# Kernel tuning notes

Measured on AMD Instinct MI355X. Metric: run time of the kernel, lower is better.

## Reference

```python
import jax, jax.numpy as jnp
import numpy as np

HEADS = 12
D_MODEL = 768
D_K = D_MODEL // HEADS


def setup_inputs() -> dict:
    key = jax.random.key(0)
    ks = jax.random.split(key, 5)
    B, S = 2, 2048
    scale = 1.0 / np.sqrt(D_MODEL)
    return {
        "q": jax.random.normal(ks[0], (B, S, D_MODEL), dtype=jnp.float32),
        "k": jax.random.normal(ks[1], (B, S, D_MODEL), dtype=jnp.float32),
        "v": jax.random.normal(ks[2], (B, S, D_MODEL), dtype=jnp.float32),
        "Wk": jax.random.normal(ks[3], (D_MODEL, D_MODEL), dtype=jnp.float32) * scale,
        "bk": jnp.zeros((D_MODEL,), dtype=jnp.float32),
        "Wo": jax.random.normal(ks[4], (D_MODEL, D_MODEL), dtype=jnp.float32) * scale,
        "bo": jnp.zeros((D_MODEL,), dtype=jnp.float32),
    }


def reference(q, k, v, Wk, bk, Wo, bo):
    B, S, _ = q.shape
    # NOTE: faithful to source bug: q, k, v ALL projected with k_linear.
    def proj(x):
        y = x @ Wk.T + bk                    # [B,S,D]
        return y.reshape(B, -1, HEADS, D_K).transpose(0, 2, 1, 3)  # [B,H,S,Dk]

    qh, kh, vh = proj(q), proj(k), proj(v)
    scores = jnp.einsum('bhsd,bhtd->bhst', qh, kh) / jnp.sqrt(jnp.float32(D_K))
    attn = jax.nn.softmax(scores, axis=-1)   # dropout is identity in eval
    out = jnp.einsum('bhst,bhtd->bhsd', attn, vh)
    concat = out.transpose(0, 2, 1, 3).reshape(B, -1, D_MODEL)
    return concat @ Wo.T + bo
```

## Files before the change

kernel.cpp:

```cpp
#include <hip/hip_runtime.h>
#include <hip/hip_bf16.h>
#include <stddef.h>

#define HEADS 12
#define DM 768
#define DK 64
#define SEQ 2048
#define NB 2
#define WSZ (DM * DM)
#define QSCALE 0.18033688011112043f

typedef __attribute__((ext_vector_type(8))) short short8;
typedef __attribute__((ext_vector_type(4))) float f32x4;

#define MFMA16(A, B, C) __builtin_amdgcn_mfma_f32_16x16x32_bf16((A), (B), (C), 0, 0, 0)

__device__ __forceinline__ unsigned short f2bf(float x) {
  union { float f; unsigned u; } c;
  c.f = x;
  unsigned r = (c.u + 0x7FFFu + ((c.u >> 16) & 1u)) >> 16;
  return (unsigned short)r;
}
__device__ __forceinline__ float bf2f(unsigned short h) {
  union { float f; unsigned u; } c;
  c.u = ((unsigned)h) << 16;
  return c.f;
}

__device__ __forceinline__ void async16(const void* g, void* l) {
  __builtin_amdgcn_global_load_lds(
      (const __attribute__((address_space(1))) void*)g,
      (__attribute__((address_space(3))) void*)l, 16, 0, 0);
}

__device__ __forceinline__ void splitpk(float a, float b, unsigned& hu, unsigned& lu) {
  union { __hip_bfloat162 v; unsigned u; } c;
  c.v = __float22bfloat162_rn(make_float2(a, b));
  hu = c.u;
  const float ra = a - bf2f((unsigned short)(hu & 0xFFFFu));
  const float rb = b - bf2f((unsigned short)(hu >> 16));
  c.v = __float22bfloat162_rn(make_float2(ra, rb));
  lu = c.u;
}
__device__ __forceinline__ unsigned pk2bf(float a, float b) {
  union { __hip_bfloat162 v; unsigned u; } c;
  c.v = __float22bfloat162_rn(make_float2(a, b));
  return c.u;
}


__global__ __launch_bounds__(256) void prep_split(
    const float* __restrict__ q, const float* __restrict__ k,
    const float* __restrict__ v, const float* __restrict__ Wk,
    const float* __restrict__ Wo, unsigned short* __restrict__ xq,
    unsigned short* __restrict__ xk, unsigned short* __restrict__ xv,
    unsigned short* __restrict__ wkh, unsigned short* __restrict__ wkl,
    unsigned short* __restrict__ woh, unsigned short* __restrict__ wol) {
  __shared__ __align__(16) unsigned short Lh[64 * 136];
  __shared__ __align__(16) unsigned short Ll[64 * 136];
  const int tid = threadIdx.x;
  int id = blockIdx.x;
  const float* S;
  unsigned short *H, *L = nullptr;
  int RT, RT16;
  if (id < 1152) {
    S = (id < 384) ? q : (id < 768) ? k : v;
    H = (id < 384) ? xq : (id < 768) ? xk : xv;
    id = id % 384; RT = 64; RT16 = 256;
  } else if (id < 1224) {
    S = Wk; H = wkh; L = wkl; id -= 1152; RT = 12; RT16 = 48;
  } else {
    S = Wo; H = woh; L = wol; id -= 1224; RT = 12; RT16 = 48;
  }
  const int rb = id % RT, kb = id / RT;
  const int mlane = tid >> 4;
  const int klane = (tid & 15) * 8;

#pragma unroll
  for (int rr = 0; rr < 4; ++rr) {
    const int m = rr * 16 + mlane;
    const float* src = &S[(size_t)(rb * 64 + m) * DM + kb * 128 + klane];
    float a[8];
    *(float4*)&a[0] = *(const float4*)&src[0];
    *(float4*)&a[4] = *(const float4*)&src[4];
    if (L) {
      unsigned hu[4], lu[4];
#pragma unroll
      for (int u = 0; u < 4; ++u) splitpk(a[2 * u], a[2 * u + 1], hu[u], lu[u]);
      *(uint4*)&Lh[m * 136 + klane] = *(uint4*)&hu[0];
      *(uint4*)&Ll[m * 136 + klane] = *(uint4*)&lu[0];
    } else {
      unsigned hu[4];
#pragma unroll
      for (int u = 0; u < 4; ++u) hu[u] = pk2bf(a[2 * u], a[2 * u + 1]);
      *(uint4*)&Lh[m * 136 + klane] = *(uint4*)&hu[0];
    }
  }
  __syncthreads();

  const int t = tid >> 4;
  const int ktp = t >> 2, mtp = t & 3;
  const size_t gt = ((size_t)(kb * 4 + ktp) * RT16 + (rb * 4 + mtp)) * 512;
#pragma unroll
  for (int i = 0; i < 4; ++i) {
    const int c = i * 16 + (tid & 15);
    const int lsrc = (mtp * 16 + (tid & 15)) * 136 + ktp * 32 + i * 8;
    *(uint4*)&H[gt + c * 8] = *(uint4*)&Lh[lsrc];
    if (L) *(uint4*)&L[gt + c * 8] = *(uint4*)&Ll[lsrc];
  }
}

__global__ __launch_bounds__(256, 3) void gemm_proj(
    const unsigned short* __restrict__ Xq, const unsigned short* __restrict__ Xk,
    const unsigned short* __restrict__ Xv, const unsigned short* __restrict__ Bh_,
    const unsigned short* __restrict__ Bl_, const float* __restrict__ bias,
    unsigned short* __restrict__ q_h, unsigned short* __restrict__ q_l,
    unsigned short* __restrict__ k_h, unsigned short* __restrict__ vt_h) {
  __shared__ __align__(16) unsigned short Ash[8 * 512];
  __shared__ __align__(16) unsigned short Bsh[6 * 512];
  __shared__ __align__(16) unsigned short Bsl[6 * 512];

  const int tid = threadIdx.x, z = blockIdx.z;
  const unsigned short* __restrict__ A = (z == 0) ? Xq : (z == 1) ? Xk : Xv;
  const int id = blockIdx.x;
  const int mt0 = (id & 31) * 8, nt0 = (id >> 5) * 6;
  const int lane = tid & 63, wv = tid >> 6;
  const int l15 = lane & 15, quad = lane >> 4;
  const int wm = (wv >> 1) * 4, wn = (wv & 1) * 3;
  const int lx = lane * 8;

  f32x4 acc[4][3];
#pragma unroll
  for (int i = 0; i < 4; ++i)
#pragma unroll
    for (int j = 0; j < 3; ++j) acc[i][j] = (f32x4){0.f, 0.f, 0.f, 0.f};

  for (int kt = 0; kt < 24; ++kt) {
    __syncthreads();
    async16(&A[((size_t)kt * 256 + mt0 + wv) * 512 + lx], &Ash[wv * 512]);
    async16(&A[((size_t)kt * 256 + mt0 + wv + 4) * 512 + lx], &Ash[(wv + 4) * 512]);
    async16(&Bh_[((size_t)kt * 48 + nt0 + wv) * 512 + lx], &Bsh[wv * 512]);
    async16(&Bl_[((size_t)kt * 48 + nt0 + wv) * 512 + lx], &Bsl[wv * 512]);
    if (wv < 2)
      async16(&Bh_[((size_t)kt * 48 + nt0 + 4 + wv) * 512 + lx], &Bsh[(4 + wv) * 512]);
    else
      async16(&Bl_[((size_t)kt * 48 + nt0 + 2 + wv) * 512 + lx], &Bsl[(2 + wv) * 512]);
    __syncthreads();

    short8 bh8[3], bl8[3];
#pragma unroll
    for (int nt = 0; nt < 3; ++nt) {
      bh8[nt] = *(const short8*)&Bsh[(wn + nt) * 512 + lx];
      bl8[nt] = *(const short8*)&Bsl[(wn + nt) * 512 + lx];
    }
#pragma unroll
    for (int mt = 0; mt < 4; ++mt) {
      const short8 ah8 = *(const short8*)&Ash[(wm + mt) * 512 + lx];
#pragma unroll
      for (int nt = 0; nt < 3; ++nt) {
        acc[mt][nt] = MFMA16(ah8, bh8[nt], acc[mt][nt]);
        acc[mt][nt] = MFMA16(ah8, bl8[nt], acc[mt][nt]);
      }
    }
  }

#pragma unroll
  for (int mt = 0; mt < 4; ++mt)
#pragma unroll
    for (int nt = 0; nt < 3; ++nt) {
      const int n = (nt0 + wn + nt) * 16 + l15;
      const float bv = bias[n];
      const int hh = n >> 6, dk = n & 63;
#pragma unroll
      for (int j = 0; j < 4; ++j) {
        const int m = (mt0 + wm + mt) * 16 + quad * 4 + j;
        const int b = m >> 11, t = m & 2047;
        const int bh = b * HEADS + hh;
        if (z == 0) {
          const float y = (acc[mt][nt][j] + bv) * QSCALE;
          const unsigned short yh = f2bf(y);
          const int a = (bh * SEQ + t) * DK + dk;
          q_h[a] = yh;
          q_l[a] = f2bf(y - bf2f(yh));
        } else if (z == 1) {
          const int a = bh * 131072 + (dk >> 5) * 65536 + (t >> 4) * 512 +
                        (((dk & 31) >> 3) * 16 + (t & 15)) * 8 + (dk & 7);
          k_h[a] = f2bf(acc[mt][nt][j] + bv);
        } else {
          const int a = bh * 131072 + (t >> 5) * 2048 + (dk >> 4) * 512 +
                        (((t & 31) >> 3) * 16 + (dk & 15)) * 8 + (t & 7);
          vt_h[a] = f2bf(acc[mt][nt][j] + bv);
        }
      }
    }
}

__global__ __launch_bounds__(256, 2) void gemm_out(
    const unsigned short* __restrict__ Ah_, const unsigned short* __restrict__ Al_,
    const unsigned short* __restrict__ Bh_, const unsigned short* __restrict__ Bl_,
    const float* __restrict__ bias, float* __restrict__ outF) {
  __shared__ __align__(16) unsigned short Ash[4 * 512];
  __shared__ __align__(16) unsigned short Asl[4 * 512];
  __shared__ __align__(16) unsigned short Bsh[6 * 512];
  __shared__ __align__(16) unsigned short Bsl[6 * 512];

  const int tid = threadIdx.x, id = blockIdx.x;
  const int mt0 = (id & 63) * 4, nt0 = (id >> 6) * 6;
  const int lane = tid & 63, wv = tid >> 6;
  const int l15 = lane & 15, quad = lane >> 4;
  const int wm = (wv >> 1) * 2, wn = (wv & 1) * 3;
  const int lx = lane * 8;

  f32x4 acc[2][3];
#pragma unroll
  for (int i = 0; i < 2; ++i)
#pragma unroll
    for (int j = 0; j < 3; ++j) acc[i][j] = (f32x4){0.f, 0.f, 0.f, 0.f};

  for (int kt = 0; kt < 24; ++kt) {
    __syncthreads();
    async16(&Ah_[((size_t)kt * 256 + mt0 + wv) * 512 + lx], &Ash[wv * 512]);
    async16(&Al_[((size_t)kt * 256 + mt0 + wv) * 512 + lx], &Asl[wv * 512]);
    async16(&Bh_[((size_t)kt * 48 + nt0 + wv) * 512 + lx], &Bsh[wv * 512]);
    async16(&Bl_[((size_t)kt * 48 + nt0 + wv) * 512 + lx], &Bsl[wv * 512]);
    if (wv < 2)
      async16(&Bh_[((size_t)kt * 48 + nt0 + 4 + wv) * 512 + lx], &Bsh[(4 + wv) * 512]);
    else
      async16(&Bl_[((size_t)kt * 48 + nt0 + 2 + wv) * 512 + lx], &Bsl[(2 + wv) * 512]);
    __syncthreads();

    short8 bh8[3], bl8[3];
#pragma unroll
    for (int nt = 0; nt < 3; ++nt) {
      bh8[nt] = *(const short8*)&Bsh[(wn + nt) * 512 + lx];
      bl8[nt] = *(const short8*)&Bsl[(wn + nt) * 512 + lx];
    }
#pragma unroll
    for (int mt = 0; mt < 2; ++mt) {
      const short8 ah8 = *(const short8*)&Ash[(wm + mt) * 512 + lx];
      const short8 al8 = *(const short8*)&Asl[(wm + mt) * 512 + lx];
#pragma unroll
      for (int nt = 0; nt < 3; ++nt) {
        acc[mt][nt] = MFMA16(ah8, bh8[nt], acc[mt][nt]);
        acc[mt][nt] = MFMA16(al8, bh8[nt], acc[mt][nt]);
        acc[mt][nt] = MFMA16(ah8, bl8[nt], acc[mt][nt]);
      }
    }
  }

#pragma unroll
  for (int mt = 0; mt < 2; ++mt)
#pragma unroll
    for (int nt = 0; nt < 3; ++nt) {
      const int n = (nt0 + wn + nt) * 16 + l15;
      const float bv = bias[n];
#pragma unroll
      for (int j = 0; j < 4; ++j) {
        const int m = (mt0 + wm + mt) * 16 + quad * 4 + j;
        outF[(size_t)m * DM + n] = acc[mt][nt][j] + bv;
      }
    }
}

__global__ __launch_bounds__(256, 3) void attn_mfma(
    const unsigned short* __restrict__ q_h, const unsigned short* __restrict__ q_l,
    const unsigned short* __restrict__ k_h, const unsigned short* __restrict__ vt_h,
    unsigned short* __restrict__ cch, unsigned short* __restrict__ ccl) {
  __shared__ __align__(16) unsigned short Ks[8 * 512];
  __shared__ __align__(16) unsigned short Vs[8 * 512];
  __shared__ __align__(16) unsigned short Ps[4 * 1024];
  __shared__ float Osh[64 * 68];
  __shared__ float Lred[4][2][16];

  const int tid = threadIdx.x, lane = tid & 63, wv = tid >> 6;
  const int l15 = lane & 15, quad = lane >> 4;
  const int qh = wv & 1, th = wv >> 1;
  const int id = blockIdx.x;
  const int bh = id % 24, q0 = (id / 24) << 6;
  const int lx = lane * 8;

  short8 Qf[2][2][2];
#pragma unroll
  for (int qt = 0; qt < 2; ++qt)
#pragma unroll
    for (int ks = 0; ks < 2; ++ks) {
      const int off =
          (bh * SEQ + q0 + qh * 32 + qt * 16 + l15) * DK + ks * 32 + quad * 8;
      Qf[qt][ks][0] = *(const short8*)&q_h[off];
      Qf[qt][ks][1] = *(const short8*)&q_l[off];
    }

  f32x4 O[2][4];
#pragma unroll
  for (int i = 0; i < 2; ++i)
#pragma unroll
    for (int j = 0; j < 4; ++j) O[i][j] = (f32x4){0.f, 0.f, 0.f, 0.f};
  float lsum[2] = {0.f, 0.f};

  const size_t kbase = (size_t)bh * 131072;
  const size_t vbase = (size_t)bh * 131072;

  for (int t0 = 0; t0 < SEQ; t0 += 64) {
    __syncthreads();
    async16(&k_h[kbase + ((size_t)(t0 >> 4) + wv) * 512 + lx], &Ks[wv * 512]);
    async16(&k_h[kbase + 65536 + ((size_t)(t0 >> 4) + wv) * 512 + lx],
            &Ks[(4 + wv) * 512]);
    async16(&vt_h[vbase + (size_t)(t0 >> 5) * 2048 + wv * 512 + lx],
            &Vs[wv * 512]);
    async16(&vt_h[vbase + ((size_t)(t0 >> 5) + 1) * 2048 + wv * 512 + lx],
            &Vs[(4 + wv) * 512]);
    __syncthreads();

    f32x4 St[2][2];
#pragma unroll
    for (int i = 0; i < 2; ++i)
#pragma unroll
      for (int j = 0; j < 2; ++j) St[i][j] = (f32x4){0.f, 0.f, 0.f, 0.f};
#pragma unroll
    for (int ks = 0; ks < 2; ++ks)
#pragma unroll
      for (int tt = 0; tt < 2; ++tt) {
        const short8 kh8 = *(const short8*)&Ks[(ks * 4 + th * 2 + tt) * 512 + lx];
#pragma unroll
        for (int qt = 0; qt < 2; ++qt) {
          St[tt][qt] = MFMA16(kh8, Qf[qt][ks][0], St[tt][qt]);
          St[tt][qt] = MFMA16(kh8, Qf[qt][ks][1], St[tt][qt]);
        }
      }

#pragma unroll
    for (int tt = 0; tt < 2; ++tt)
#pragma unroll
      for (int qt = 0; qt < 2; ++qt) {
        const float p0 = __builtin_amdgcn_exp2f(fminf(St[tt][qt][0], 40.f));
        const float p1 = __builtin_amdgcn_exp2f(fminf(St[tt][qt][1], 40.f));
        const float p2 = __builtin_amdgcn_exp2f(fminf(St[tt][qt][2], 40.f));
        const float p3 = __builtin_amdgcn_exp2f(fminf(St[tt][qt][3], 40.f));
        lsum[qt] += (p0 + p1) + (p2 + p3);
        unsigned pk[2];
        pk[0] = pk2bf(p0, p1);
        pk[1] = pk2bf(p2, p3);
        *(uint2*)&Ps[wv * 1024 + qt * 512 +
                     ((2 * tt + (quad >> 1)) * 16 + l15) * 8 + (quad & 1) * 4] =
            *(uint2*)&pk[0];
      }
    asm volatile("s_waitcnt lgkmcnt(0)" ::: "memory");

    short8 pf[2];
#pragma unroll
    for (int qt = 0; qt < 2; ++qt)
      pf[qt] = *(const short8*)&Ps[wv * 1024 + qt * 512 + lx];
#pragma unroll
    for (int nt = 0; nt < 4; ++nt) {
      const short8 vh8 = *(const short8*)&Vs[(th * 4 + nt) * 512 + lx];
      O[0][nt] = MFMA16(pf[0], vh8, O[0][nt]);
      O[1][nt] = MFMA16(pf[1], vh8, O[1][nt]);
    }
  }

#pragma unroll
  for (int qt = 0; qt < 2; ++qt) {
    float l = lsum[qt];
    l += __shfl_xor(l, 16);
    l += __shfl_xor(l, 32);
    if (quad == 0) Lred[wv][qt][l15] = l;
  }
  __syncthreads();
  if (th == 1) {
#pragma unroll
    for (int qt = 0; qt < 2; ++qt)
#pragma unroll
      for (int nt = 0; nt < 4; ++nt)
#pragma unroll
        for (int j = 0; j < 4; ++j)
          Osh[(qh * 32 + qt * 16 + quad * 4 + j) * 68 + nt * 16 + l15] =
              O[qt][nt][j];
  }
  __syncthreads();
  if (th == 0) {
    const int b = bh / HEADS, hh = bh % HEADS;
#pragma unroll
    for (int qt = 0; qt < 2; ++qt)
#pragma unroll
      for (int j = 0; j < 4; ++j) {
        const int qloc = qh * 32 + qt * 16 + quad * 4 + j;
        const float inv = 1.0f / (Lred[wv][qt][quad * 4 + j] +
                                  Lred[wv + 2][qt][quad * 4 + j]);
        const int m = b * SEQ + q0 + qloc;
#pragma unroll
        for (int nt = 0; nt < 4; ++nt) {
          const float y = (O[qt][nt][j] + Osh[qloc * 68 + nt * 16 + l15]) * inv;
          const int kk = hh * 64 + nt * 16 + l15;
          const int a = ((kk >> 5) * 256 + (m >> 4)) * 512 +
                        (((kk & 31) >> 3) * 16 + (m & 15)) * 8 + (kk & 7);
          const unsigned short yh = f2bf(y);
          cch[a] = yh;
          ccl[a] = f2bf(y - bf2f(yh));
        }
      }
  }
}

extern "C" void kernel_launch(void* const* d_in, const int* in_sizes, int n_in,
                              void* d_out, int out_size, void* d_ws,
                              size_t ws_size, hipStream_t stream) {
  const float* q = (const float*)d_in[0];
  const float* k = (const float*)d_in[1];
  const float* v = (const float*)d_in[2];
  const float* Wk = (const float*)d_in[3];
  const float* bk = (const float*)d_in[4];
  const float* Wo = (const float*)d_in[5];
  const float* bo = (const float*)d_in[6];
  float* out = (float*)d_out;

  const size_t SZ = (size_t)NB * SEQ * DM;
  unsigned short* ws16 = (unsigned short*)d_ws;
  unsigned short* xq = ws16;
  unsigned short* xk = ws16 + SZ;
  unsigned short* xv = ws16 + 2 * SZ;
  unsigned short* cch = xq;
  unsigned short* ccl = xk;
  unsigned short* qp_h = ws16 + 3 * SZ;
  unsigned short* qp_l = ws16 + 4 * SZ;
  unsigned short* kp = ws16 + 5 * SZ;
  unsigned short* vtp = ws16 + 6 * SZ;
  unsigned short* wkh = ws16 + 7 * SZ;
  unsigned short* wkl = wkh + WSZ;
  unsigned short* woh = wkl + WSZ;
  unsigned short* wol = woh + WSZ;

  prep_split<<<dim3(1296), 256, 0, stream>>>(q, k, v, Wk, Wo, xq, xk, xv, wkh,
                                             wkl, woh, wol);
  gemm_proj<<<dim3(256, 1, 3), 256, 0, stream>>>(xq, xk, xv, wkh, wkl, bk,
                                                 qp_h, qp_l, kp, vtp);
  attn_mfma<<<dim3(768), 256, 0, stream>>>(qp_h, qp_l, kp, vtp, cch, ccl);
  gemm_out<<<dim3(512), 256, 0, stream>>>(cch, ccl, woh, wol, bo, out);
}
```

Before: 203.7 us.

## Double-buffer K/V tiles in attention loop with async prefetch and MFMA priority

The attention loop now keeps two LDS buffers for K/V. It issues the async copy for the next tile before computing the current one, so global loads overlap with MFMA and softmax work. The full __syncthreads pair is replaced by a vmcnt wait plus raw barriers, and s_setprio raises wave priority around the MFMA blocks. The staging buffers are unioned with the output-reduction scratch to keep LDS usage bounded. The last iteration issues a wasted prefetch that wraps to tile 0, and correctness now depends on the hand-placed waitcnt/barrier ordering.

```diff
diff --git a/kernel.cpp b/kernel.cpp
--- a/kernel.cpp
+++ b/kernel.cpp
@@ -266,10 +266,11 @@
     const unsigned short* __restrict__ q_h, const unsigned short* __restrict__ q_l,
     const unsigned short* __restrict__ k_h, const unsigned short* __restrict__ vt_h,
     unsigned short* __restrict__ cch, unsigned short* __restrict__ ccl) {
-  __shared__ __align__(16) unsigned short Ks[8 * 512];
-  __shared__ __align__(16) unsigned short Vs[8 * 512];
+  __shared__ __align__(16) union {
+    unsigned short stage[2][16 * 512];
+    float osh[64 * 68];
+  } sm;
   __shared__ __align__(16) unsigned short Ps[4 * 1024];
-  __shared__ float Osh[64 * 68];
   __shared__ float Lred[4][2][16];
 
   const int tid = threadIdx.x, lane = tid & 63, wv = tid >> 6;
@@ -297,25 +298,38 @@
     for (int j = 0; j < 4; ++j) O[i][j] = (f32x4){0.f, 0.f, 0.f, 0.f};
   float lsum[2] = {0.f, 0.f};
 
-  const size_t kbase = (size_t)bh * 131072;
-  const size_t vbase = (size_t)bh * 131072;
-
+  const unsigned short* __restrict__ kbh = k_h + (size_t)bh * 131072;
+  const unsigned short* __restrict__ vbh = vt_h + (size_t)bh * 131072;
+
+#define STAGE(T0S, BUF)                                                          \
+  do {                                                                           \
+    unsigned short* Ksb_ = &sm.stage[(BUF)][0];                                  \
+    unsigned short* Vsb_ = &sm.stage[(BUF)][8 * 512];                            \
+    async16(&kbh[((size_t)((T0S) >> 4) + wv) * 512 + lx], &Ksb_[wv * 512]);      \
+    async16(&kbh[65536 + ((size_t)((T0S) >> 4) + wv) * 512 + lx],                \
+            &Ksb_[(4 + wv) * 512]);                                              \
+    async16(&vbh[(size_t)((T0S) >> 5) * 2048 + wv * 512 + lx],                   \
+            &Vsb_[wv * 512]);                                                    \
+    async16(&vbh[((size_t)((T0S) >> 5) + 1) * 2048 + wv * 512 + lx],             \
+            &Vsb_[(4 + wv) * 512]);                                              \
+  } while (0)
+
+  STAGE(0, 0);
+  int cur = 0;
   for (int t0 = 0; t0 < SEQ; t0 += 64) {
-    __syncthreads();
-    async16(&k_h[kbase + ((size_t)(t0 >> 4) + wv) * 512 + lx], &Ks[wv * 512]);
-    async16(&k_h[kbase + 65536 + ((size_t)(t0 >> 4) + wv) * 512 + lx],
-            &Ks[(4 + wv) * 512]);
-    async16(&vt_h[vbase + (size_t)(t0 >> 5) * 2048 + wv * 512 + lx],
-            &Vs[wv * 512]);
-    async16(&vt_h[vbase + ((size_t)(t0 >> 5) + 1) * 2048 + wv * 512 + lx],
-            &Vs[(4 + wv) * 512]);
-    __syncthreads();
+    STAGE((t0 + 64) & (SEQ - 1), cur ^ 1);
+    asm volatile("s_waitcnt vmcnt(4)" ::: "memory");
+    asm volatile("s_barrier" ::: "memory");
+
+    const unsigned short* Ks = &sm.stage[cur][0];
+    const unsigned short* Vs = &sm.stage[cur][8 * 512];
 
     f32x4 St[2][2];
 #pragma unroll
     for (int i = 0; i < 2; ++i)
 #pragma unroll
       for (int j = 0; j < 2; ++j) St[i][j] = (f32x4){0.f, 0.f, 0.f, 0.f};
+    __builtin_amdgcn_s_setprio(1);
 #pragma unroll
     for (int ks = 0; ks < 2; ++ks)
 #pragma unroll
@@ -327,6 +341,7 @@
           St[tt][qt] = MFMA16(kh8, Qf[qt][ks][1], St[tt][qt]);
         }
       }
+    __builtin_amdgcn_s_setprio(0);
 
 #pragma unroll
     for (int tt = 0; tt < 2; ++tt)
@@ -350,13 +365,19 @@
 #pragma unroll
     for (int qt = 0; qt < 2; ++qt)
       pf[qt] = *(const short8*)&Ps[wv * 1024 + qt * 512 + lx];
+    __builtin_amdgcn_s_setprio(1);
 #pragma unroll
     for (int nt = 0; nt < 4; ++nt) {
       const short8 vh8 = *(const short8*)&Vs[(th * 4 + nt) * 512 + lx];
       O[0][nt] = MFMA16(pf[0], vh8, O[0][nt]);
       O[1][nt] = MFMA16(pf[1], vh8, O[1][nt]);
     }
-  }
+    __builtin_amdgcn_s_setprio(0);
+
+    asm volatile("s_barrier" ::: "memory");
+    cur ^= 1;
+  }
+#undef STAGE
 
 #pragma unroll
   for (int qt = 0; qt < 2; ++qt) {
@@ -365,6 +386,7 @@
     l += __shfl_xor(l, 32);
     if (quad == 0) Lred[wv][qt][l15] = l;
   }
+  asm volatile("s_waitcnt vmcnt(0)" ::: "memory");
   __syncthreads();
   if (th == 1) {
 #pragma unroll
@@ -373,7 +395,7 @@
       for (int nt = 0; nt < 4; ++nt)
 #pragma unroll
         for (int j = 0; j < 4; ++j)
-          Osh[(qh * 32 + qt * 16 + quad * 4 + j) * 68 + nt * 16 + l15] =
+          sm.osh[(qh * 32 + qt * 16 + quad * 4 + j) * 68 + nt * 16 + l15] =
               O[qt][nt][j];
   }
   __syncthreads();
@@ -389,7 +411,7 @@
         const int m = b * SEQ + q0 + qloc;
 #pragma unroll
         for (int nt = 0; nt < 4; ++nt) {
-          const float y = (O[qt][nt][j] + Osh[qloc * 68 + nt * 16 + l15]) * inv;
+          const float y = (O[qt][nt][j] + sm.osh[qloc * 68 + nt * 16 + l15]) * inv;
           const int kk = hh * 64 + nt * 16 + l15;
           const int a = ((kk >> 5) * 256 + (m >> 4)) * 512 +
                         (((kk & 31) >> 3) * 16 + (m & 15)) * 8 + (kk & 7);
```

Result: no change. 202.6 us (-0.5%).
